# Optimization experiments

Measured on AMD Instinct MI355X. Metric: run time of the kernel, lower is better.

The kernel has to match this reference:

```python
import jax, jax.numpy as jnp
import numpy as np

N, NFEAT, NHID, NCLASS = 8192, 512, 256, 16
ALPHA = 0.01          # LeakyReLU negative slope
NEG = -9.0e15         # mask fill value from the original code
ADJ_DENSITY = 0.01    # ~82 neighbors per node


def setup_inputs() -> dict:
    key = jax.random.key(0)
    ks = jax.random.split(key, 9)
    x = jax.random.normal(ks[0], (N, NFEAT), jnp.float32)
    # sparse binary adjacency with self-loops, stored dense as in the torch code
    adj = (jax.random.uniform(ks[1], (N, N)) < ADJ_DENSITY).astype(jnp.int32)
    adj = adj.at[jnp.arange(N), jnp.arange(N)].set(1)
    s = 0.05
    W1 = jax.random.normal(ks[2], (NFEAT, NHID), jnp.float32) * s   # gc1.weight
    b1 = jax.random.normal(ks[3], (NHID,), jnp.float32) * s         # gc1.bias
    Wa = jax.random.normal(ks[4], (NHID, NHID), jnp.float32) * s    # out_att.W (nhid*nheads -> nhid)
    a_vec = jax.random.normal(ks[5], (2 * NHID, 1), jnp.float32) * s  # out_att.a
    W3 = jax.random.normal(ks[6], (NHID, NCLASS), jnp.float32) * s  # gc3.weight
    b3 = jax.random.normal(ks[7], (NCLASS,), jnp.float32) * s       # gc3.bias
    return {"x": x, "adj": adj, "W1": W1, "b1": b1, "Wa": Wa,
            "a_vec": a_vec, "W3": W3, "b3": b3}


def reference(x, adj, W1, b1, Wa, a_vec, W3, b3):
    adjf = adj.astype(x.dtype)
    # gc1: spmm(adj, x @ W1) + b1, then ReLU  (eval mode -> dropout is identity)
    h1 = jax.nn.relu(adjf @ (x @ W1) + b1)        # [N, NHID]
    feat = h1
    # out_att (GraphAttentionLayer, concat=False)
    Wh = h1 @ Wa                                   # [N, NHID]
    f1 = Wh @ a_vec[:NHID]                         # [N, 1]
    f2 = Wh @ a_vec[NHID:]                         # [N, 1]
    e = jax.nn.leaky_relu(f1 + f2.T, ALPHA)        # dense [N, N] scores
    e = jnp.where(adj > 0, e, jnp.asarray(NEG, x.dtype))
    attention = jax.nn.softmax(e, axis=1)          # row-wise masked softmax
    h_prime = attention @ Wh                       # [N, NHID]
    a_out = jax.nn.elu(h_prime)                    # x = F.elu(a)
    # gc3
    out = adjf @ (a_out @ W3) + b3                 # [N, NCLASS]
    return (jax.nn.sigmoid(out), attention, jnp.concatenate([feat, out], axis=1))
```

## Files before the change

### kernel.cpp

```cpp
#include <hip/hip_runtime.h>
#include <hip/hip_bf16.h>

#define NN    8192
#define NFEAT 512
#define NHID  256
#define NCLASS 16
#define ELLW  256
#define CONVB 2048

typedef __hip_bfloat16 bf16;
typedef unsigned short u16;
typedef __bf16 bf16x8 __attribute__((ext_vector_type(8)));
typedef float  f32x4  __attribute__((ext_vector_type(4)));
typedef int    i32x4  __attribute__((ext_vector_type(4)));

__device__ inline float bf2f(u16 u) { return __uint_as_float(((unsigned int)u) << 16); }
__device__ inline u16 f2bfu(float f) {
  bf16 b = __float2bfloat16(f);
  u16 u;
  __builtin_memcpy(&u, &b, 2);
  return u;
}

__device__ inline int nanhits(unsigned w) {
  return ((((w >> 7) & 0xFF) == 0xFF) ? 1 : 0) + ((((w >> 23) & 0xFF) == 0xFF) ? 1 : 0);
}

__global__ __launch_bounds__(256) void probe_dtype2(const uint4* __restrict__ a, int nchunks_a,
                                                    const uint4* __restrict__ b, int nchunks_b,
                                                    int* __restrict__ cnt) {
  int c = 0;
  int gid = blockIdx.x * 256 + threadIdx.x;
  int stride = gridDim.x * 256;
  for (int i = gid; i < nchunks_a; i += stride * 4) {
    uint4 v = a[i];
    c += nanhits(v.x) + nanhits(v.y) + nanhits(v.z) + nanhits(v.w);
  }
  for (int i = gid; i < nchunks_b; i += stride) {
    uint4 v = b[i];
    c += nanhits(v.x) + nanhits(v.y) + nanhits(v.z) + nanhits(v.w);
  }
  if (c) atomicAdd(cnt, c);
}

__global__ __launch_bounds__(256) void prep_all(const int* __restrict__ adj,
                                                int* __restrict__ ell_cnt,
                                                u16* __restrict__ ell_col,
                                                const void* __restrict__ x_raw,
                                                const void* __restrict__ W1r,
                                                const void* __restrict__ War,
                                                const void* __restrict__ b1r,
                                                const void* __restrict__ avr,
                                                const void* __restrict__ W3r,
                                                const void* __restrict__ b3r,
                                                bf16* __restrict__ xc,
                                                bf16* __restrict__ W1t,
                                                bf16* __restrict__ Wat,
                                                float* __restrict__ b1f,
                                                float* __restrict__ avecf,
                                                float* __restrict__ W3f,
                                                float* __restrict__ b3f,
                                                float* __restrict__ f12a,
                                                const int* __restrict__ flagcnt,
                                                int mode) {
  __shared__ int cnt;
  int b = blockIdx.x;
  if (b < NN) {
    int row = b;
    if (threadIdx.x == 0) cnt = 0;
    __syncthreads();
    const i32x4* arow = (const i32x4*)(adj + (size_t)row * NN);
    u16* crow = ell_col + (size_t)row * ELLW;
    int lane = threadIdx.x & 63;
    unsigned long long lt = ((unsigned long long)1 << lane) - 1;
    for (int j4 = threadIdx.x; j4 < NN / 4; j4 += 256) {
      i32x4 v = __builtin_nontemporal_load(&arow[j4]);
      unsigned long long m0 = __ballot(v.x != 0);
      unsigned long long m1 = __ballot(v.y != 0);
      unsigned long long m2 = __ballot(v.z != 0);
      unsigned long long m3 = __ballot(v.w != 0);
      int c0 = __popcll(m0), c1 = __popcll(m1), c2 = __popcll(m2), c3 = __popcll(m3);
      int total = c0 + c1 + c2 + c3;
      int base = 0;
      if (lane == 0 && total) base = atomicAdd(&cnt, total);
      base = __shfl(base, 0, 64);
      int col = j4 * 4;
      if (v.x) { int p = base + __popcll(m0 & lt);                 if (p < ELLW) crow[p] = (u16)col;       }
      if (v.y) { int p = base + c0 + __popcll(m1 & lt);            if (p < ELLW) crow[p] = (u16)(col + 1); }
      if (v.z) { int p = base + c0 + c1 + __popcll(m2 & lt);       if (p < ELLW) crow[p] = (u16)(col + 2); }
      if (v.w) { int p = base + c0 + c1 + c2 + __popcll(m3 & lt);  if (p < ELLW) crow[p] = (u16)(col + 3); }
    }
    __syncthreads();
    if (threadIdx.x == 0) ell_cnt[row] = cnt < ELLW ? cnt : ELLW;
  } else {
    int cb = b - NN;
    bool isf32 = (mode < 0) ? (*flagcnt > 16) : (mode != 0);
    auto rd = [&](const void* p, int i) -> float {
      return isf32 ? ((const float*)p)[i] : __bfloat162float(((const bf16*)p)[i]);
    };
    int gid = cb * 256 + threadIdx.x;
    const int gstride = CONVB * 256;
    for (int i = gid; i < 2 * NN; i += gstride) f12a[i] = 0.f;
    const int n4x = NN * NFEAT / 4;
    const int n1 = NFEAT * NHID;
    const int n2 = n1 + NHID * NHID;
    const int n3 = n2 + NHID;
    const int n4 = n3 + 2 * NHID;
    const int n5 = n4 + NHID * NCLASS;
    const int n6 = n5 + NCLASS;
    const int total = n4x + n6;
    for (int i = gid; i < total; i += gstride) {
      if (i < n4x) {
        ushort4 o;
        if (isf32) {
          f32x4 v = ((const f32x4*)x_raw)[i];
          o.x = f2bfu(v.x); o.y = f2bfu(v.y); o.z = f2bfu(v.z); o.w = f2bfu(v.w);
        } else {
          o = ((const ushort4*)x_raw)[i];
        }
        ((ushort4*)xc)[i] = o;
      } else {
        int j = i - n4x;
        if (j < n1)      { int k = j / NHID, n = j % NHID; W1t[(size_t)n * NFEAT + k] = __float2bfloat16(rd(W1r, j)); }
        else if (j < n2) { int q = j - n1; int k = q / NHID, n = q % NHID; Wat[(size_t)n * NHID + k] = __float2bfloat16(rd(War, q)); }
        else if (j < n3) b1f[j - n2] = rd(b1r, j - n2);
        else if (j < n4) avecf[j - n3] = rd(avr, j - n3);
        else if (j < n5) W3f[j - n4] = rd(W3r, j - n4);
        else             b3f[j - n5] = rd(b3r, j - n5);
      }
    }
  }
}

#define TM 64
#define TN 64
#define LDSP 72

__global__ __launch_bounds__(256) void gemm_bt(const bf16* __restrict__ A, int lda,
                                               const bf16* __restrict__ Bt, int ldb,
                                               bf16* __restrict__ C, int ldc, int K,
                                               const float* __restrict__ avec,
                                               float* __restrict__ f12) {
  __shared__ __align__(16) bf16 sA[TM * LDSP];
  __shared__ __align__(16) bf16 sB[TN * LDSP];
  int bm = blockIdx.x, bn = blockIdx.y;
  int t = threadIdx.x;
  int wave = t >> 6, lane = t & 63;
  int quad = lane >> 4, l16 = lane & 15;
  f32x4 acc[4] = {};

  int srow = t >> 2;
  int sk   = (t & 3) * 16;
  const size_t abase = (size_t)(bm * TM + srow) * lda + sk;
  const size_t bbase = (size_t)(bn * TN + srow) * ldb + sk;

  uint4 pa0 = *(const uint4*)&A[abase];
  uint4 pa1 = *(const uint4*)&A[abase + 8];
  uint4 pb0 = *(const uint4*)&Bt[bbase];
  uint4 pb1 = *(const uint4*)&Bt[bbase + 8];

  for (int kt = 0; kt < K; kt += 64) {
    *(uint4*)&sA[srow * LDSP + sk]     = pa0;
    *(uint4*)&sA[srow * LDSP + sk + 8] = pa1;
    *(uint4*)&sB[srow * LDSP + sk]     = pb0;
    *(uint4*)&sB[srow * LDSP + sk + 8] = pb1;
    __syncthreads();
    if (kt + 64 < K) {
      pa0 = *(const uint4*)&A[abase + kt + 64];
      pa1 = *(const uint4*)&A[abase + kt + 72];
      pb0 = *(const uint4*)&Bt[bbase + kt + 64];
      pb1 = *(const uint4*)&Bt[bbase + kt + 72];
    }
    bf16x8 af0 = *(const bf16x8*)&sA[(wave * 16 + l16) * LDSP + quad * 8];
    bf16x8 af1 = *(const bf16x8*)&sA[(wave * 16 + l16) * LDSP + 32 + quad * 8];
#pragma unroll
    for (int c = 0; c < 4; ++c) {
      bf16x8 bf0 = *(const bf16x8*)&sB[(c * 16 + l16) * LDSP + quad * 8];
      bf16x8 bf1 = *(const bf16x8*)&sB[(c * 16 + l16) * LDSP + 32 + quad * 8];
      acc[c] = __builtin_amdgcn_mfma_f32_16x16x32_bf16(af0, bf0, acc[c], 0, 0, 0);
      acc[c] = __builtin_amdgcn_mfma_f32_16x16x32_bf16(af1, bf1, acc[c], 0, 0, 0);
    }
    __syncthreads();
  }
  int row0 = bm * TM + wave * 16 + quad * 4;
  int col0 = bn * TN;
#pragma unroll
  for (int c = 0; c < 4; ++c) {
#pragma unroll
    for (int r = 0; r < 4; ++r) {
      C[(size_t)(row0 + r) * ldc + col0 + c * 16 + l16] = __float2bfloat16(acc[c][r]);
    }
  }
  if (f12) {
    float av1[4], av2[4];
#pragma unroll
    for (int c = 0; c < 4; ++c) {
      int col = col0 + c * 16 + l16;
      av1[c] = avec[col];
      av2[c] = avec[NHID + col];
    }
#pragma unroll
    for (int r = 0; r < 4; ++r) {
      float s1 = 0.f, s2 = 0.f;
#pragma unroll
      for (int c = 0; c < 4; ++c) {
        s1 += acc[c][r] * av1[c];
        s2 += acc[c][r] * av2[c];
      }
      for (int m = 1; m <= 8; m <<= 1) {
        s1 += __shfl_xor(s1, m, 64);
        s2 += __shfl_xor(s2, m, 64);
      }
      if (l16 == 0) {
        atomicAdd(&f12[row0 + r], s1);
        atomicAdd(&f12[NN + row0 + r], s2);
      }
    }
  }
}

__global__ __launch_bounds__(256) void spmm_h1(const bf16* __restrict__ XW,
                                               const int* __restrict__ ell_cnt,
                                               const u16* __restrict__ ell_col,
                                               const float* __restrict__ b1,
                                               float* __restrict__ out2,
                                               bf16* __restrict__ h1b) {
  __shared__ int sc[4][ELLW];
  int wave = threadIdx.x >> 6, lane = threadIdx.x & 63;
  int row = blockIdx.x * 4 + wave;
  int nn = ell_cnt[row];
  const u16* cr = ell_col + (size_t)row * ELLW;
  for (int k = lane; k < nn; k += 64) sc[wave][k] = cr[k];
  float a0 = 0.f, a1 = 0.f, a2 = 0.f, a3 = 0.f;
  const int c0 = lane * 4;
#pragma unroll 4
  for (int k = 0; k < nn; ++k) {
    ushort4 v = *(const ushort4*)&XW[(size_t)sc[wave][k] * NHID + c0];
    a0 += bf2f(v.x); a1 += bf2f(v.y); a2 += bf2f(v.z); a3 += bf2f(v.w);
  }
  f32x4 bb = *(const f32x4*)&b1[c0];
  a0 = fmaxf(a0 + bb.x, 0.f);
  a1 = fmaxf(a1 + bb.y, 0.f);
  a2 = fmaxf(a2 + bb.z, 0.f);
  a3 = fmaxf(a3 + bb.w, 0.f);
  f32x4 r; r.x = a0; r.y = a1; r.z = a2; r.w = a3;
  *(f32x4*)&out2[(size_t)row * (NHID + NCLASS) + c0] = r;
  ushort4 h; h.x = f2bfu(a0); h.y = f2bfu(a1); h.z = f2bfu(a2); h.w = f2bfu(a3);
  *(ushort4*)&h1b[(size_t)row * NHID + c0] = h;
}

__global__ __launch_bounds__(256) void attn_fused(const bf16* __restrict__ Wh,
                                                  const int* __restrict__ ell_cnt,
                                                  const u16* __restrict__ ell_col,
                                                  const float* __restrict__ f12,
                                                  const float* __restrict__ W3,
                                                  float* __restrict__ att,
                                                  bf16* __restrict__ aout,
                                                  float* __restrict__ A3) {
  __shared__ __align__(16) float rowbuf[NN];
  __shared__ float p[ELLW];
  __shared__ int scols[ELLW];
  __shared__ float red[8];
  __shared__ __align__(16) float hacc[4][NHID];
  int row = blockIdx.x, t = threadIdx.x;
  int wave = t >> 6, lane = t & 63;
  int nn = ell_cnt[row];
  const u16* cr = ell_col + (size_t)row * ELLW;
  float f1i = f12[row];
  const float* f2 = f12 + NN;

  f32x4* rb4 = (f32x4*)rowbuf;
  f32x4 z = {0.f, 0.f, 0.f, 0.f};
#pragma unroll
  for (int k = t; k < NN / 4; k += 256) rb4[k] = z;
  for (int k = t; k < nn; k += 256) scols[k] = cr[k];
  __syncthreads();

  float lmax = -1e30f;
  for (int k = t; k < nn; k += 256) {
    float e = f1i + f2[scols[k]];
    e = (e > 0.f) ? e : 0.01f * e;
    p[k] = e;
    lmax = fmaxf(lmax, e);
  }
  for (int o = 32; o > 0; o >>= 1) lmax = fmaxf(lmax, __shfl_down(lmax, o, 64));
  if (lane == 0) red[wave] = lmax;
  __syncthreads();
  float gmax = fmaxf(fmaxf(red[0], red[1]), fmaxf(red[2], red[3]));

  float lsum = 0.f;
  for (int k = t; k < nn; k += 256) {
    float ex = __expf(p[k] - gmax);
    p[k] = ex;
    lsum += ex;
  }
  for (int o = 32; o > 0; o >>= 1) lsum += __shfl_down(lsum, o, 64);
  __syncthreads();
  if (lane == 0) red[4 + wave] = lsum;
  __syncthreads();
  float inv = 1.f / fmaxf(red[4] + red[5] + red[6] + red[7], 1e-30f);

  for (int k = t; k < nn; k += 256) rowbuf[scols[k]] = p[k] * inv;

  const int c0 = lane * 4;
  float a0 = 0.f, a1 = 0.f, a2 = 0.f, a3 = 0.f;
#pragma unroll 4
  for (int k = wave; k < nn; k += 4) {
    float pk = p[k];
    ushort4 v = *(const ushort4*)&Wh[(size_t)scols[k] * NHID + c0];
    a0 += pk * bf2f(v.x);
    a1 += pk * bf2f(v.y);
    a2 += pk * bf2f(v.z);
    a3 += pk * bf2f(v.w);
  }
  f32x4 pa; pa.x = a0; pa.y = a1; pa.z = a2; pa.w = a3;
  *(f32x4*)&hacc[wave][c0] = pa;
  __syncthreads();

  f32x4* dst = (f32x4*)(att + (size_t)row * NN);
#pragma unroll
  for (int k = t; k < NN / 4; k += 256) __builtin_nontemporal_store(rb4[k], &dst[k]);

  float s = (hacc[0][t] + hacc[1][t] + hacc[2][t] + hacc[3][t]) * inv;
  float e = (s > 0.f) ? s : (__expf(s) - 1.f);
  aout[(size_t)row * NHID + t] = __float2bfloat16(e);

  p[t] = e;
  __syncthreads();
  {
    int cc = t & 15, g = t >> 4, k0 = g * 16;
    float part = 0.f;
#pragma unroll
    for (int j = 0; j < 16; ++j)
      part += p[k0 + j] * W3[(k0 + j) * NCLASS + cc];
    float* parts = (float*)scols;
    parts[t] = part;
    __syncthreads();
    if (t < NCLASS) {
      float s3 = 0.f;
#pragma unroll
      for (int g2 = 0; g2 < 16; ++g2) s3 += parts[g2 * 16 + t];
      A3[(size_t)row * NCLASS + t] = s3;
    }
  }
}

__global__ __launch_bounds__(256) void attn_sparse(const bf16* __restrict__ Wh,
                                                   const int* __restrict__ ell_cnt,
                                                   const u16* __restrict__ ell_col,
                                                   const float* __restrict__ f12,
                                                   bf16* __restrict__ aout) {
  __shared__ float p[ELLW];
  __shared__ int scols[ELLW];
  __shared__ float red[8];
  int row = blockIdx.x, t = threadIdx.x;
  int nn = ell_cnt[row];
  const u16* cr = ell_col + (size_t)row * ELLW;
  float f1i = f12[row];
  const float* f2 = f12 + NN;
  for (int k = t; k < nn; k += 256) scols[k] = cr[k];
  __syncthreads();
  float lmax = -1e30f;
  for (int k = t; k < nn; k += 256) {
    float e = f1i + f2[scols[k]];
    e = (e > 0.f) ? e : 0.01f * e;
    p[k] = e;
    lmax = fmaxf(lmax, e);
  }
  for (int o = 32; o > 0; o >>= 1) lmax = fmaxf(lmax, __shfl_down(lmax, o, 64));
  if ((t & 63) == 0) red[t >> 6] = lmax;
  __syncthreads();
  float gmax = fmaxf(fmaxf(red[0], red[1]), fmaxf(red[2], red[3]));
  float lsum = 0.f;
  for (int k = t; k < nn; k += 256) {
    float ex = __expf(p[k] - gmax);
    p[k] = ex;
    lsum += ex;
  }
  for (int o = 32; o > 0; o >>= 1) lsum += __shfl_down(lsum, o, 64);
  __syncthreads();
  if ((t & 63) == 0) red[4 + (t >> 6)] = lsum;
  __syncthreads();
  float inv = 1.f / fmaxf(red[4] + red[5] + red[6] + red[7], 1e-30f);
  float acc = 0.f;
  for (int k = 0; k < nn; ++k)
    acc += p[k] * __bfloat162float(Wh[(size_t)scols[k] * NHID + t]);
  acc *= inv;
  float e = (acc > 0.f) ? acc : (__expf(acc) - 1.f);
  aout[(size_t)row * NHID + t] = __float2bfloat16(e);
}

__global__ __launch_bounds__(256) void attn_dense(const int* __restrict__ adj,
                                                  const float* __restrict__ f12,
                                                  float* __restrict__ att) {
  __shared__ __align__(16) float rowbuf[NN];
  __shared__ float se[ELLW];
  __shared__ int sj[ELLW];
  __shared__ float red[8];
  __shared__ int cnt;
  int row = blockIdx.x, t = threadIdx.x;
  if (t == 0) cnt = 0;
  f32x4* rb4 = (f32x4*)rowbuf;
  f32x4 z = {0.f, 0.f, 0.f, 0.f};
  for (int k = t; k < NN / 4; k += 256) rb4[k] = z;
  float f1i = f12[row];
  const float* f2 = f12 + NN;
  __syncthreads();
  const int4* arow = (const int4*)(adj + (size_t)row * NN);
  for (int j4 = t; j4 < NN / 4; j4 += 256) {
    int4 v = arow[j4];
    int base = j4 * 4;
    if (v.x) { int p = atomicAdd(&cnt, 1); if (p < ELLW) { sj[p] = base;     se[p] = f1i + f2[base];     } }
    if (v.y) { int p = atomicAdd(&cnt, 1); if (p < ELLW) { sj[p] = base + 1; se[p] = f1i + f2[base + 1]; } }
    if (v.z) { int p = atomicAdd(&cnt, 1); if (p < ELLW) { sj[p] = base + 2; se[p] = f1i + f2[base + 2]; } }
    if (v.w) { int p = atomicAdd(&cnt, 1); if (p < ELLW) { sj[p] = base + 3; se[p] = f1i + f2[base + 3]; } }
  }
  __syncthreads();
  int nn = cnt < ELLW ? cnt : ELLW;
  float lmax = -1e30f;
  for (int k = t; k < nn; k += 256) {
    float e = se[k];
    e = (e > 0.f) ? e : 0.01f * e;
    se[k] = e;
    lmax = fmaxf(lmax, e);
  }
  for (int o = 32; o > 0; o >>= 1) lmax = fmaxf(lmax, __shfl_down(lmax, o, 64));
  if ((t & 63) == 0) red[t >> 6] = lmax;
  __syncthreads();
  float gmax = fmaxf(fmaxf(red[0], red[1]), fmaxf(red[2], red[3]));
  float lsum = 0.f;
  for (int k = t; k < nn; k += 256) {
    float ex = __expf(se[k] - gmax);
    se[k] = ex;
    lsum += ex;
  }
  for (int o = 32; o > 0; o >>= 1) lsum += __shfl_down(lsum, o, 64);
  __syncthreads();
  if ((t & 63) == 0) red[4 + (t >> 6)] = lsum;
  __syncthreads();
  float inv = 1.f / fmaxf(red[4] + red[5] + red[6] + red[7], 1e-30f);
  for (int k = t; k < nn; k += 256) rowbuf[sj[k]] = se[k] * inv;
  __syncthreads();
  const f32x4* src = (const f32x4*)rowbuf;
  f32x4* dst = (f32x4*)(att + (size_t)row * NN);
  for (int k = t; k < NN / 4; k += 256) dst[k] = src[k];
}

__global__ __launch_bounds__(256) void gemm3(const bf16* __restrict__ aout,
                                             const float* __restrict__ W3,
                                             float* __restrict__ A3) {
  __shared__ float sW[NHID * NCLASS];
  __shared__ bf16 sa[16 * NHID];
  int t = threadIdx.x;
  for (int k = t; k < NHID * NCLASS; k += 256) sW[k] = W3[k];
  int r0 = blockIdx.x * 16;
  for (int k = t; k < 16 * NHID; k += 256) sa[k] = aout[(size_t)r0 * NHID + k];
  __syncthreads();
  int r = t >> 4, c = t & 15;
  float acc = 0.f;
#pragma unroll 8
  for (int k = 0; k < NHID; ++k)
    acc += __bfloat162float(sa[r * NHID + k]) * sW[k * NCLASS + c];
  A3[(size_t)(r0 + r) * NCLASS + c] = acc;
}

__global__ __launch_bounds__(256) void spmm_out2(const float* __restrict__ A3,
                                                 const int* __restrict__ ell_cnt,
                                                 const u16* __restrict__ ell_col,
                                                 const float* __restrict__ b3,
                                                 float* __restrict__ out2,
                                                 float* __restrict__ out0,
                                                 int write_sig) {
  int g = blockIdx.x * 256 + threadIdx.x;
  int row = g >> 4, c = g & 15;
  int nn = ell_cnt[row];
  const u16* cr = ell_col + (size_t)row * ELLW;
  float acc = b3[c];
#pragma unroll 8
  for (int k = 0; k < nn; ++k)
    acc += A3[(size_t)cr[k] * NCLASS + c];
  out2[(size_t)row * (NHID + NCLASS) + NHID + c] = acc;
  if (write_sig) out0[g] = 1.f / (1.f + __expf(-acc));
}

__global__ __launch_bounds__(256) void copy_f32(const float* __restrict__ src,
                                                float* __restrict__ dst, int n) {
  int i = blockIdx.x * 256 + threadIdx.x;
  if (i < n) dst[i] = src[i];
}

__global__ __launch_bounds__(256) void sigmoid_from_out2(const float* __restrict__ out2,
                                                         float* __restrict__ out0) {
  int g = blockIdx.x * 256 + threadIdx.x;
  int row = g >> 4, c = g & 15;
  float v = out2[(size_t)row * (NHID + NCLASS) + NHID + c];
  out0[g] = 1.f / (1.f + __expf(-v));
}

extern "C" void kernel_launch(void* const* d_in, const int* in_sizes, int n_in,
                              void* d_out, int out_size, void* d_ws, size_t ws_size,
                              hipStream_t stream) {
  const void* x_raw    = d_in[0];
  const int*  adj      = (const int*)d_in[1];
  const void* W1_raw   = d_in[2];
  const void* b1_raw   = d_in[3];
  const void* Wa_raw   = d_in[4];
  const void* avec_raw = d_in[5];
  const void* W3_raw   = d_in[6];
  const void* b3_raw   = d_in[7];

  float* out0 = (float*)d_out;
  float* out1 = out0 + (size_t)NN * NCLASS;
  float* out2 = out1 + (size_t)NN * NN;

  const size_t NEED = 36u << 20;
  bool useWS = (d_ws != nullptr) && (ws_size >= NEED);

  char* a = useWS ? (char*)d_ws : (char*)out1;
  size_t o = 0;
  auto carve = [&](size_t bytes) { char* p = a + o; o += (bytes + 4095) & ~(size_t)4095; return p; };
  int*   flag    = (int*)  carve(4096);
  int*   ell_cnt = (int*)  carve((size_t)NN * 4);
  u16*   ell_col = (u16*)  carve((size_t)NN * ELLW * 2);
  bf16*  xc      = (bf16*) carve((size_t)NN * NFEAT * 2);
  bf16*  W1t     = (bf16*) carve((size_t)NHID * NFEAT * 2);
  bf16*  Wat     = (bf16*) carve((size_t)NHID * NHID * 2);
  float* avecf   = (float*)carve((size_t)2 * NHID * 4);
  float* b1f     = (float*)carve((size_t)NHID * 4);
  float* b3f     = (float*)carve((size_t)NCLASS * 4);
  float* W3f     = (float*)carve((size_t)NHID * NCLASS * 4);
  bf16*  XW      = (bf16*) carve((size_t)NN * NHID * 2);
  bf16*  h1b     = (bf16*) carve((size_t)NN * NHID * 2);
  bf16*  Wh      = (bf16*) carve((size_t)NN * NHID * 2);
  float* f12a    = (float*)carve((size_t)2 * NN * 4);
  bf16*  aout    = (bf16*) carve((size_t)NN * NHID * 2);
  float* A3ws    = (float*)carve((size_t)NN * NCLASS * 4);

  float* A3 = useWS ? A3ws : out0;
  float* f12stash = out0;

  int mode;
  {
    long long sx = in_sizes ? (long long)in_sizes[0] : -1;
    long long sw = in_sizes ? (long long)in_sizes[2] : -1;
    int mx = (sx == (long long)NN * NFEAT * 4) ? 1 : (sx == (long long)NN * NFEAT * 2 ? 0 : -1);
    int mw = (sw == (long long)NFEAT * NHID * 4) ? 1 : (sw == (long long)NFEAT * NHID * 2 ? 0 : -1);
    mode = (mx >= 0 && mx == mw) ? mx : -1;
  }
  if (mode < 0) {
    (void)hipMemsetAsync(flag, 0, 4, stream);
    probe_dtype2<<<256, 256, 0, stream>>>((const uint4*)x_raw, NN * NFEAT / 8,
                                          (const uint4*)W1_raw, NFEAT * NHID / 8, flag);
  }

  prep_all<<<NN + CONVB, 256, 0, stream>>>(adj, ell_cnt, ell_col,
                                           x_raw, W1_raw, Wa_raw, b1_raw, avec_raw, W3_raw, b3_raw,
                                           xc, W1t, Wat, b1f, avecf, W3f, b3f,
                                           f12a, flag, mode);
  gemm_bt<<<dim3(NN / TM, NHID / TN), 256, 0, stream>>>(xc, NFEAT, W1t, NFEAT, XW, NHID, NFEAT,
                                                        nullptr, nullptr);
  spmm_h1<<<NN / 4, 256, 0, stream>>>(XW, ell_cnt, ell_col, b1f, out2, h1b);
  gemm_bt<<<dim3(NN / TM, NHID / TN), 256, 0, stream>>>(h1b, NHID, Wat, NHID, Wh, NHID, NHID,
                                                        avecf, f12a);

  if (useWS) {
    attn_fused<<<NN, 256, 0, stream>>>(Wh, ell_cnt, ell_col, f12a, W3f, out1, aout, A3);
    spmm_out2<<<NN * NCLASS / 256, 256, 0, stream>>>(A3, ell_cnt, ell_col, b3f, out2, out0, 1);
  } else {
    attn_sparse<<<NN, 256, 0, stream>>>(Wh, ell_cnt, ell_col, f12a, aout);
    gemm3<<<NN / 16, 256, 0, stream>>>(aout, W3f, A3);
    spmm_out2<<<NN * NCLASS / 256, 256, 0, stream>>>(A3, ell_cnt, ell_col, b3f, out2, out0, 0);
    copy_f32<<<(2 * NN + 255) / 256, 256, 0, stream>>>(f12a, f12stash, 2 * NN);
    attn_dense<<<NN, 256, 0, stream>>>(adj, f12stash, out1);
    sigmoid_from_out2<<<NN * NCLASS / 256, 256, 0, stream>>>(out2, out0);
  }
}
```

Before: 523.8 us.

## Overlap ELL construction with first GEMM and split x/W1 conversion

```diff
diff --git a/kernel.cpp b/kernel.cpp
--- a/kernel.cpp
+++ b/kernel.cpp
@@ -6,7 +6,6 @@
 #define NHID  256
 #define NCLASS 16
 #define ELLW  256
-#define CONVB 2048
 
 typedef __hip_bfloat16 bf16;
 typedef unsigned short u16;
@@ -43,26 +42,154 @@
   if (c) atomicAdd(cnt, c);
 }
 
-__global__ __launch_bounds__(256) void prep_all(const int* __restrict__ adj,
-                                                int* __restrict__ ell_cnt,
-                                                u16* __restrict__ ell_col,
-                                                const void* __restrict__ x_raw,
-                                                const void* __restrict__ W1r,
-                                                const void* __restrict__ War,
-                                                const void* __restrict__ b1r,
-                                                const void* __restrict__ avr,
-                                                const void* __restrict__ W3r,
-                                                const void* __restrict__ b3r,
-                                                bf16* __restrict__ xc,
-                                                bf16* __restrict__ W1t,
-                                                bf16* __restrict__ Wat,
-                                                float* __restrict__ b1f,
-                                                float* __restrict__ avecf,
-                                                float* __restrict__ W3f,
-                                                float* __restrict__ b3f,
-                                                float* __restrict__ f12a,
-                                                const int* __restrict__ flagcnt,
-                                                int mode) {
+__global__ __launch_bounds__(256) void convert_xW1(const void* __restrict__ x_raw,
+                                                   const void* __restrict__ W1r,
+                                                   bf16* __restrict__ xc,
+                                                   bf16* __restrict__ W1t,
+                                                   const int* __restrict__ flagcnt,
+                                                   int mode) {
+  bool isf32 = (mode < 0) ? (*flagcnt > 16) : (mode != 0);
+  const int n4x = NN * NFEAT / 4;
+  const int n1 = NFEAT * NHID;
+  const int total = n4x + n1;
+  for (int i = blockIdx.x * 256 + threadIdx.x; i < total; i += gridDim.x * 256) {
+    if (i < n4x) {
+      ushort4 o;
+      if (isf32) {
+        f32x4 v = ((const f32x4*)x_raw)[i];
+        o.x = f2bfu(v.x); o.y = f2bfu(v.y); o.z = f2bfu(v.z); o.w = f2bfu(v.w);
+      } else {
+        o = ((const ushort4*)x_raw)[i];
+      }
+      ((ushort4*)xc)[i] = o;
+    } else {
+      int j = i - n4x;
+      int k = j / NHID, n = j % NHID;
+      float v = isf32 ? ((const float*)W1r)[j] : __bfloat162float(((const bf16*)W1r)[j]);
+      W1t[(size_t)n * NFEAT + k] = __float2bfloat16(v);
+    }
+  }
+}
+
+#define TM 64
+#define TN 64
+#define LDSP 72
+
+__device__ __forceinline__ void gemm_tile(int bm, int bn,
+                                          const bf16* __restrict__ A, int lda,
+                                          const bf16* __restrict__ Bt, int ldb,
+                                          bf16* __restrict__ C, int ldc, int K,
+                                          const float* __restrict__ avec,
+                                          float* __restrict__ f12,
+                                          bf16* sA, bf16* sB) {
+  int t = threadIdx.x;
+  int wave = t >> 6, lane = t & 63;
+  int quad = lane >> 4, l16 = lane & 15;
+  f32x4 acc[4] = {};
+
+  int srow = t >> 2;
+  int sk   = (t & 3) * 16;
+  const size_t abase = (size_t)(bm * TM + srow) * lda + sk;
+  const size_t bbase = (size_t)(bn * TN + srow) * ldb + sk;
+
+  uint4 pa0 = *(const uint4*)&A[abase];
+  uint4 pa1 = *(const uint4*)&A[abase + 8];
+  uint4 pb0 = *(const uint4*)&Bt[bbase];
+  uint4 pb1 = *(const uint4*)&Bt[bbase + 8];
+
+  for (int kt = 0; kt < K; kt += 64) {
+    *(uint4*)&sA[srow * LDSP + sk]     = pa0;
+    *(uint4*)&sA[srow * LDSP + sk + 8] = pa1;
+    *(uint4*)&sB[srow * LDSP + sk]     = pb0;
+    *(uint4*)&sB[srow * LDSP + sk + 8] = pb1;
+    __syncthreads();
+    if (kt + 64 < K) {
+      pa0 = *(const uint4*)&A[abase + kt + 64];
+      pa1 = *(const uint4*)&A[abase + kt + 72];
+      pb0 = *(const uint4*)&Bt[bbase + kt + 64];
+      pb1 = *(const uint4*)&Bt[bbase + kt + 72];
+    }
+    bf16x8 af0 = *(const bf16x8*)&sA[(wave * 16 + l16) * LDSP + quad * 8];
+    bf16x8 af1 = *(const bf16x8*)&sA[(wave * 16 + l16) * LDSP + 32 + quad * 8];
+#pragma unroll
+    for (int c = 0; c < 4; ++c) {
+      bf16x8 bf0 = *(const bf16x8*)&sB[(c * 16 + l16) * LDSP + quad * 8];
+      bf16x8 bf1 = *(const bf16x8*)&sB[(c * 16 + l16) * LDSP + 32 + quad * 8];
+      acc[c] = __builtin_amdgcn_mfma_f32_16x16x32_bf16(af0, bf0, acc[c], 0, 0, 0);
+      acc[c] = __builtin_amdgcn_mfma_f32_16x16x32_bf16(af1, bf1, acc[c], 0, 0, 0);
+    }
+    __syncthreads();
+  }
+  int row0 = bm * TM + wave * 16 + quad * 4;
+  int col0 = bn * TN;
+#pragma unroll
+  for (int c = 0; c < 4; ++c) {
+#pragma unroll
+    for (int r = 0; r < 4; ++r) {
+      C[(size_t)(row0 + r) * ldc + col0 + c * 16 + l16] = __float2bfloat16(acc[c][r]);
+    }
+  }
+  if (f12) {
+    float av1[4], av2[4];
+#pragma unroll
+    for (int c = 0; c < 4; ++c) {
+      int col = col0 + c * 16 + l16;
+      av1[c] = avec[col];
+      av2[c] = avec[NHID + col];
+    }
+#pragma unroll
+    for (int r = 0; r < 4; ++r) {
+      float s1 = 0.f, s2 = 0.f;
+#pragma unroll
+      for (int c = 0; c < 4; ++c) {
+        s1 += acc[c][r] * av1[c];
+        s2 += acc[c][r] * av2[c];
+      }
+      for (int m = 1; m <= 8; m <<= 1) {
+        s1 += __shfl_xor(s1, m, 64);
+        s2 += __shfl_xor(s2, m, 64);
+      }
+      if (l16 == 0) {
+        atomicAdd(&f12[row0 + r], s1);
+        atomicAdd(&f12[NN + row0 + r], s2);
+      }
+    }
+  }
+}
+
+__global__ __launch_bounds__(256) void gemm_bt(const bf16* __restrict__ A, int lda,
+                                               const bf16* __restrict__ Bt, int ldb,
+                                               bf16* __restrict__ C, int ldc, int K,
+                                               const float* __restrict__ avec,
+                                               float* __restrict__ f12) {
+  __shared__ __align__(16) bf16 sAB[2 * TM * LDSP];
+  gemm_tile(blockIdx.x, blockIdx.y, A, lda, Bt, ldb, C, ldc, K, avec, f12,
+            sAB, sAB + TM * LDSP);
+}
+
+#define GB1 ((NN / TM) * (NHID / TN))
+#define CVB 64
+
+__global__ __launch_bounds__(256) void ell_gemm1(const int* __restrict__ adj,
+                                                 int* __restrict__ ell_cnt,
+                                                 u16* __restrict__ ell_col,
+                                                 const bf16* __restrict__ xc,
+                                                 const bf16* __restrict__ W1t,
+                                                 bf16* __restrict__ XW,
+                                                 const void* __restrict__ War,
+                                                 const void* __restrict__ b1r,
+                                                 const void* __restrict__ avr,
+                                                 const void* __restrict__ W3r,
+                                                 const void* __restrict__ b3r,
+                                                 bf16* __restrict__ Wat,
+                                                 float* __restrict__ b1f,
+                                                 float* __restrict__ avecf,
+                                                 float* __restrict__ W3f,
+                                                 float* __restrict__ b3f,
+                                                 float* __restrict__ f12a,
+                                                 const int* __restrict__ flagcnt,
+                                                 int mode) {
+  __shared__ __align__(16) bf16 sAB[2 * TM * LDSP];
   __shared__ int cnt;
   int b = blockIdx.x;
   if (b < NN) {
@@ -92,129 +219,31 @@
     }
     __syncthreads();
     if (threadIdx.x == 0) ell_cnt[row] = cnt < ELLW ? cnt : ELLW;
+  } else if (b < NN + GB1) {
+    int cb = b - NN;
+    int bm = cb % (NN / TM), bn = cb / (NN / TM);
+    gemm_tile(bm, bn, xc, NFEAT, W1t, NFEAT, XW, NHID, NFEAT, nullptr, nullptr,
+              sAB, sAB + TM * LDSP);
   } else {
-    int cb = b - NN;
+    int cb = b - NN - GB1;
     bool isf32 = (mode < 0) ? (*flagcnt > 16) : (mode != 0);
     auto rd = [&](const void* p, int i) -> float {
       return isf32 ? ((const float*)p)[i] : __bfloat162float(((const bf16*)p)[i]);
     };
     int gid = cb * 256 + threadIdx.x;
-    const int gstride = CONVB * 256;
+    const int gstride = CVB * 256;
     for (int i = gid; i < 2 * NN; i += gstride) f12a[i] = 0.f;
-    const int n4x = NN * NFEAT / 4;
-    const int n1 = NFEAT * NHID;
-    const int n2 = n1 + NHID * NHID;
+    const int n2 = NHID * NHID;
     const int n3 = n2 + NHID;
     const int n4 = n3 + 2 * NHID;
     const int n5 = n4 + NHID * NCLASS;
     const int n6 = n5 + NCLASS;
-    const int total = n4x + n6;
-    for (int i = gid; i < total; i += gstride) {
-      if (i < n4x) {
-        ushort4 o;
-        if (isf32) {
-          f32x4 v = ((const f32x4*)x_raw)[i];
-          o.x = f2bfu(v.x); o.y = f2bfu(v.y); o.z = f2bfu(v.z); o.w = f2bfu(v.w);
-        } else {
-          o = ((const ushort4*)x_raw)[i];
-        }
-        ((ushort4*)xc)[i] = o;
-      } else {
-        int j = i - n4x;
-        if (j < n1)      { int k = j / NHID, n = j % NHID; W1t[(size_t)n * NFEAT + k] = __float2bfloat16(rd(W1r, j)); }
-        else if (j < n2) { int q = j - n1; int k = q / NHID, n = q % NHID; Wat[(size_t)n * NHID + k] = __float2bfloat16(rd(War, q)); }
-        else if (j < n3) b1f[j - n2] = rd(b1r, j - n2);
-        else if (j < n4) avecf[j - n3] = rd(avr, j - n3);
-        else if (j < n5) W3f[j - n4] = rd(W3r, j - n4);
-        else             b3f[j - n5] = rd(b3r, j - n5);
-      }
-    }
-  }
-}
-
-#define TM 64
-#define TN 64
-#define LDSP 72
-
-__global__ __launch_bounds__(256) void gemm_bt(const bf16* __restrict__ A, int lda,
-                                               const bf16* __restrict__ Bt, int ldb,
-                                               bf16* __restrict__ C, int ldc, int K,
-                                               const float* __restrict__ avec,
-                                               float* __restrict__ f12) {
-  __shared__ __align__(16) bf16 sA[TM * LDSP];
-  __shared__ __align__(16) bf16 sB[TN * LDSP];
-  int bm = blockIdx.x, bn = blockIdx.y;
-  int t = threadIdx.x;
-  int wave = t >> 6, lane = t & 63;
-  int quad = lane >> 4, l16 = lane & 15;
-  f32x4 acc[4] = {};
-
-  int srow = t >> 2;
-  int sk   = (t & 3) * 16;
-  const size_t abase = (size_t)(bm * TM + srow) * lda + sk;
-  const size_t bbase = (size_t)(bn * TN + srow) * ldb + sk;
-
-  uint4 pa0 = *(const uint4*)&A[abase];
-  uint4 pa1 = *(const uint4*)&A[abase + 8];
-  uint4 pb0 = *(const uint4*)&Bt[bbase];
-  uint4 pb1 = *(const uint4*)&Bt[bbase + 8];
-
-  for (int kt = 0; kt < K; kt += 64) {
-    *(uint4*)&sA[srow * LDSP + sk]     = pa0;
-    *(uint4*)&sA[srow * LDSP + sk + 8] = pa1;
-    *(uint4*)&sB[srow * LDSP + sk]     = pb0;
-    *(uint4*)&sB[srow * LDSP + sk + 8] = pb1;
-    __syncthreads();
-    if (kt + 64 < K) {
-      pa0 = *(const uint4*)&A[abase + kt + 64];
-      pa1 = *(const uint4*)&A[abase + kt + 72];
-      pb0 = *(const uint4*)&Bt[bbase + kt + 64];
-      pb1 = *(const uint4*)&Bt[bbase + kt + 72];
-    }
-    bf16x8 af0 = *(const bf16x8*)&sA[(wave * 16 + l16) * LDSP + quad * 8];
-    bf16x8 af1 = *(const bf16x8*)&sA[(wave * 16 + l16) * LDSP + 32 + quad * 8];
-#pragma unroll
-    for (int c = 0; c < 4; ++c) {
-      bf16x8 bf0 = *(const bf16x8*)&sB[(c * 16 + l16) * LDSP + quad * 8];
-      bf16x8 bf1 = *(const bf16x8*)&sB[(c * 16 + l16) * LDSP + 32 + quad * 8];
-      acc[c] = __builtin_amdgcn_mfma_f32_16x16x32_bf16(af0, bf0, acc[c], 0, 0, 0);
-      acc[c] = __builtin_amdgcn_mfma_f32_16x16x32_bf16(af1, bf1, acc[c], 0, 0, 0);
-    }
-    __syncthreads();
-  }
-  int row0 = bm * TM + wave * 16 + quad * 4;
-  int col0 = bn * TN;
-#pragma unroll
-  for (int c = 0; c < 4; ++c) {
-#pragma unroll
-    for (int r = 0; r < 4; ++r) {
-      C[(size_t)(row0 + r) * ldc + col0 + c * 16 + l16] = __float2bfloat16(acc[c][r]);
-    }
-  }
-  if (f12) {
-    float av1[4], av2[4];
-#pragma unroll
-    for (int c = 0; c < 4; ++c) {
-      int col = col0 + c * 16 + l16;
-      av1[c] = avec[col];
-      av2[c] = avec[NHID + col];
-    }
-#pragma unroll
-    for (int r = 0; r < 4; ++r) {
-      float s1 = 0.f, s2 = 0.f;
-#pragma unroll
-      for (int c = 0; c < 4; ++c) {
-        s1 += acc[c][r] * av1[c];
-        s2 += acc[c][r] * av2[c];
-      }
-      for (int m = 1; m <= 8; m <<= 1) {
-        s1 += __shfl_xor(s1, m, 64);
-        s2 += __shfl_xor(s2, m, 64);
-      }
-      if (l16 == 0) {
-        atomicAdd(&f12[row0 + r], s1);
-        atomicAdd(&f12[NN + row0 + r], s2);
-      }
+    for (int j = gid; j < n6; j += gstride) {
+      if (j < n2)      { int k = j / NHID, n = j % NHID; Wat[(size_t)n * NHID + k] = __float2bfloat16(rd(War, j)); }
+      else if (j < n3) b1f[j - n2] = rd(b1r, j - n2);
+      else if (j < n4) avecf[j - n3] = rd(avr, j - n3);
+      else if (j < n5) W3f[j - n4] = rd(W3r, j - n4);
+      else             b3f[j - n5] = rd(b3r, j - n5);
     }
   }
 }
@@ -301,6 +330,11 @@
   float inv = 1.f / fmaxf(red[4] + red[5] + red[6] + red[7], 1e-30f);
 
   for (int k = t; k < nn; k += 256) rowbuf[scols[k]] = p[k] * inv;
+  __syncthreads();
+
+  f32x4* dst = (f32x4*)(att + (size_t)row * NN);
+#pragma unroll
+  for (int k = t; k < NN / 4; k += 256) __builtin_nontemporal_store(rb4[k], &dst[k]);
 
   const int c0 = lane * 4;
   float a0 = 0.f, a1 = 0.f, a2 = 0.f, a3 = 0.f;
@@ -316,10 +350,6 @@
   f32x4 pa; pa.x = a0; pa.y = a1; pa.z = a2; pa.w = a3;
   *(f32x4*)&hacc[wave][c0] = pa;
   __syncthreads();
-
-  f32x4* dst = (f32x4*)(att + (size_t)row * NN);
-#pragma unroll
-  for (int k = t; k < NN / 4; k += 256) __builtin_nontemporal_store(rb4[k], &dst[k]);
 
   float s = (hacc[0][t] + hacc[1][t] + hacc[2][t] + hacc[3][t]) * inv;
   float e = (s > 0.f) ? s : (__expf(s) - 1.f);
@@ -553,12 +583,12 @@
                                           (const uint4*)W1_raw, NFEAT * NHID / 8, flag);
   }
 
-  prep_all<<<NN + CONVB, 256, 0, stream>>>(adj, ell_cnt, ell_col,
-                                           x_raw, W1_raw, Wa_raw, b1_raw, avec_raw, W3_raw, b3_raw,
-                                           xc, W1t, Wat, b1f, avecf, W3f, b3f,
-                                           f12a, flag, mode);
-  gemm_bt<<<dim3(NN / TM, NHID / TN), 256, 0, stream>>>(xc, NFEAT, W1t, NFEAT, XW, NHID, NFEAT,
-                                                        nullptr, nullptr);
+  convert_xW1<<<2048, 256, 0, stream>>>(x_raw, W1_raw, xc, W1t, flag, mode);
+  ell_gemm1<<<NN + GB1 + CVB, 256, 0, stream>>>(adj, ell_cnt, ell_col,
+                                                xc, W1t, XW,
+                                                Wa_raw, b1_raw, avec_raw, W3_raw, b3_raw,
+                                                Wat, b1f, avecf, W3f, b3f,
+                                                f12a, flag, mode);
   spmm_h1<<<NN / 4, 256, 0, stream>>>(XW, ell_cnt, ell_col, b1f, out2, h1b);
   gemm_bt<<<dim3(NN / TM, NHID / TN), 256, 0, stream>>>(h1b, NHID, Wat, NHID, Wh, NHID, NHID,
                                                         avecf, f12a);
```

Measured after the change: 534.2 us. No clear change (+2.0%).
